# Optimization experiments

Measured on AMD Instinct MI355X. Metric: run time of the kernel, lower is better.

## Reference

```python
import jax, jax.numpy as jnp
import numpy as np

N = 100000
E = 1600000
IN_C, HID_C, OUT_C = 128, 128, 64


def setup_inputs() -> dict:
    key = jax.random.key(0)
    k_x, k_e, k_w1, k_w2 = jax.random.split(key, 4)
    x = jax.random.normal(k_x, (N, IN_C), dtype=jnp.float32)
    edge_index = jax.random.randint(k_e, (2, E), 0, N, dtype=jnp.int32)
    # nn.Linear default init: U(-1/sqrt(fan_in), 1/sqrt(fan_in)); bias init zeros per module
    lim1 = 1.0 / np.sqrt(IN_C)
    lim2 = 1.0 / np.sqrt(HID_C)
    W1 = jax.random.uniform(k_w1, (IN_C, HID_C), minval=-lim1, maxval=lim1, dtype=jnp.float32)
    b1 = jnp.zeros((HID_C,), dtype=jnp.float32)
    W2 = jax.random.uniform(k_w2, (HID_C, OUT_C), minval=-lim2, maxval=lim2, dtype=jnp.float32)
    b2 = jnp.zeros((OUT_C,), dtype=jnp.float32)
    return {"x": x, "edge_index": edge_index, "W1": W1, "b1": b1, "W2": W2, "b2": b2}


def _out_degree_gcn_conv(x, src, dst, W, b, n_nodes):
    # linear projection (no bias in lin)
    h = x @ W  # [N, out_c]
    # out-degree of each source node
    deg = jax.ops.segment_sum(jnp.ones((src.shape[0],), dtype=h.dtype), src, num_segments=n_nodes)
    deg_inv = 1.0 / jnp.maximum(deg, 1.0)  # clamp(min=1)
    h = h * deg_inv[:, None]
    # message: x_j = h[src]; aggregate: sum at dst
    out = jax.ops.segment_sum(h[src], dst, num_segments=n_nodes)  # [N, out_c]
    return out + b


def reference(x, edge_index, W1, b1, W2, b2):
    src, dst = edge_index[0], edge_index[1]
    n = x.shape[0]
    h = _out_degree_gcn_conv(x, src, dst, W1, b1, n)
    h = jax.nn.relu(h)
    # dropout p=0.0 -> identity
    out = _out_degree_gcn_conv(h, src, dst, W2, b2, n)
    return out
```

## Files before the change

### kernel.cpp

```cpp
#include <hip/hip_runtime.h>
#include <hip/hip_bf16.h>


typedef __attribute__((ext_vector_type(8))) short short8;
typedef __attribute__((ext_vector_type(4))) float floatx4;

__device__ inline unsigned short f2bf(float f) {
    union { float f; unsigned u; } v; v.f = f;
    unsigned r = v.u + 0x7FFF + ((v.u >> 16) & 1);
    return (unsigned short)(r >> 16);
}
__device__ inline float bf2f(unsigned b) {
    union { unsigned u; float f; } v; v.u = b << 16;
    return v.f;
}
__device__ inline float bf2f_hi(unsigned b) {
    union { unsigned u; float f; } v; v.u = b & 0xFFFF0000u;
    return v.f;
}

#define NBMAX 512
#define CAP   8192

__global__ __launch_bounds__(256) void convw_kernel(
    const float* __restrict__ W1, const float* __restrict__ W2,
    unsigned short* __restrict__ Wb1, unsigned short* __restrict__ Wb2,
    int* __restrict__ cnt)
{
    int i = blockIdx.x * 256 + threadIdx.x;
    if (i < NBMAX * 32) cnt[i] = 0;
    if (i < 128 * 128) {
        int k = i >> 7, n = i & 127;
        Wb1[n * 128 + k] = f2bf(W1[k * 128 + n]);
    }
    i -= 128 * 128;
    if (i >= 0 && i < 128 * 64) {
        int k = i >> 6, n = i & 63;
        Wb2[n * 128 + k] = f2bf(W2[k * 64 + n]);
    }
}

__global__ __launch_bounds__(256) void scatter2_kernel(
    const int* __restrict__ src, const int* __restrict__ dst, int E,
    int* __restrict__ cnt_d, int* __restrict__ cnt_s,
    unsigned* __restrict__ pairs, unsigned char* __restrict__ srcs_b, int NB)
{
    __shared__ int hd[NBMAX], bd[NBMAX], cd_[NBMAX];
    __shared__ int hs[NBMAX], bs[NBMAX], cs_[NBMAX];
    for (int i = threadIdx.x; i < NB; i += 256) { hd[i] = 0; cd_[i] = 0; hs[i] = 0; cs_[i] = 0; }
    __syncthreads();
    const int e0 = blockIdx.x * 8192;
    const int e1 = min(e0 + 8192, E);
    for (int i = e0 + threadIdx.x; i < e1; i += 256) {
        atomicAdd(&hd[dst[i] >> 8], 1);
        atomicAdd(&hs[src[i] >> 8], 1);
    }
    __syncthreads();
    for (int i = threadIdx.x; i < NB; i += 256) {
        if (hd[i]) bd[i] = atomicAdd(&cnt_d[i * 16], hd[i]);
        if (hs[i]) bs[i] = atomicAdd(&cnt_s[i * 16], hs[i]);
    }
    __syncthreads();
    for (int i = e0 + threadIdx.x; i < e1; i += 256) {
        int sv = src[i], dv = dst[i];
        int b = dv >> 8;
        int slot = atomicAdd(&cd_[b], 1);
        pairs[(size_t)b * CAP + bd[b] + slot] = ((unsigned)(dv & 255) << 24) | (unsigned)sv;
        int b2 = sv >> 8;
        int slot2 = atomicAdd(&cs_[b2], 1);
        srcs_b[(size_t)b2 * CAP + bs[b2] + slot2] = (unsigned char)(sv & 255);
    }
}

__global__ __launch_bounds__(256) void bucket_finalize_kernel(
    const unsigned* __restrict__ pairs, const unsigned char* __restrict__ srcs_b,
    const int* __restrict__ cnt_d, const int* __restrict__ cnt_s,
    int* __restrict__ sorted_src, int2* __restrict__ se,
    float* __restrict__ deg_inv, int N)
{
    const int b = blockIdx.x;
    const int node0 = b << 8;
    const int t = threadIdx.x;
    const size_t base = (size_t)b * CAP;
    __shared__ int hist[256];
    __shared__ int cur[256];
    __shared__ int pre[256];

    const int cd = cnt_d[b * 16];
    hist[t] = 0;
    __syncthreads();
    for (int i = t; i < cd; i += 256)
        atomicAdd(&hist[pairs[base + i] >> 24], 1);
    __syncthreads();
    int v = hist[t];
    int v4 = (v + 3) & ~3;
    pre[t] = v4;
    __syncthreads();
    for (int o = 1; o < 256; o <<= 1) {
        int add = (t >= o) ? pre[t - o] : 0;
        __syncthreads();
        pre[t] += add;
        __syncthreads();
    }
    int excl = pre[t] - v4;
    cur[t] = excl;
    if (node0 + t < N)
        se[node0 + t] = make_int2((int)base + excl, (int)base + excl + v);
    __syncthreads();
    for (int i = t; i < cd; i += 256) {
        unsigned p = pairs[base + i];
        int pos = atomicAdd(&cur[p >> 24], 1);
        sorted_src[base + pos] = (int)(p & 0xFFFFFFu);
    }

    __syncthreads();
    hist[t] = 0;
    __syncthreads();
    const int cs = cnt_s[b * 16];
    for (int i = t; i < cs; i += 256)
        atomicAdd(&hist[srcs_b[base + i]], 1);
    __syncthreads();
    if (node0 + t < N) {
        int d = hist[t];
        deg_inv[node0 + t] = 1.0f / (float)(d < 1 ? 1 : d);
    }
}

template <int NC, int AF>
__global__ __launch_bounds__(256) void gemm_mfma_kernel(
    const void* __restrict__ Ap, const unsigned short* __restrict__ Wb,
    const float* __restrict__ scale, unsigned short* __restrict__ Cb, int M)
{
    constexpr int NT = NC / 16;
    const int t = threadIdx.x;
    const int wm = t >> 6;
    const int lane = t & 63;
    const int lm = lane & 15;
    const int lk = (lane >> 4) * 8;

    const int r0 = blockIdx.x * 64 + wm * 16;
    int row = r0 + lm;
    if (row >= M) row = M - 1;

    floatx4 acc[NT];
#pragma unroll
    for (int j = 0; j < NT; ++j) acc[j] = (floatx4){0.f, 0.f, 0.f, 0.f};

#pragma unroll
    for (int kk = 0; kk < 4; ++kk) {
        const int kb = kk * 32 + lk;
        short8 af;
        if (AF) {
            const float* arow = (const float*)Ap + (size_t)row * 128 + kb;
            float4 a0 = *(const float4*)arow;
            float4 a1 = *(const float4*)(arow + 4);
            af[0] = (short)f2bf(a0.x); af[1] = (short)f2bf(a0.y);
            af[2] = (short)f2bf(a0.z); af[3] = (short)f2bf(a0.w);
            af[4] = (short)f2bf(a1.x); af[5] = (short)f2bf(a1.y);
            af[6] = (short)f2bf(a1.z); af[7] = (short)f2bf(a1.w);
        } else {
            af = *(const short8*)&((const unsigned short*)Ap)[(size_t)row * 128 + kb];
        }
#pragma unroll
        for (int j = 0; j < NT; ++j) {
            short8 bfr = *(const short8*)&Wb[(size_t)(j * 16 + lm) * 128 + kb];
            acc[j] = __builtin_amdgcn_mfma_f32_16x16x32_bf16(af, bfr, acc[j], 0, 0, 0);
        }
    }

    const int rbase = r0 + (lane >> 4) * 4;
#pragma unroll
    for (int reg = 0; reg < 4; ++reg) {
        int rg = rbase + reg;
        if (rg < M) {
            float di = AF ? scale[rg] : 1.0f;
#pragma unroll
            for (int j = 0; j < NT; ++j)
                Cb[(size_t)rg * NC + j * 16 + lm] = f2bf(AF ? acc[j][reg] * di : acc[j][reg]);
        }
    }
}

__global__ __launch_bounds__(256) void aggregate128_kernel(
    const int2* __restrict__ se, const int* __restrict__ sorted_src,
    const unsigned* __restrict__ val, const float* __restrict__ bias,
    const float* __restrict__ deg_inv, unsigned* __restrict__ outb, int N)
{
    int node = blockIdx.x * 8 + (threadIdx.x >> 5);
    if (node >= N) return;
    int l = threadIdx.x & 31;
    int2 r = se[node];
    int e = r.x;
    const int end = r.y;
    float a0 = 0.f, a1 = 0.f, a2 = 0.f, a3 = 0.f;
    if (e + 4 <= end) {
        int4 idx = *(const int4*)&sorted_src[e];
        for (; e + 8 <= end; e += 4) {
            int4 nidx = *(const int4*)&sorted_src[e + 4];
            uint2 v0 = *(const uint2*)&val[(size_t)idx.x * 64 + 2 * l];
            uint2 v1 = *(const uint2*)&val[(size_t)idx.y * 64 + 2 * l];
            uint2 v2 = *(const uint2*)&val[(size_t)idx.z * 64 + 2 * l];
            uint2 v3 = *(const uint2*)&val[(size_t)idx.w * 64 + 2 * l];
            a0 += (bf2f(v0.x & 0xFFFF) + bf2f(v1.x & 0xFFFF)) + (bf2f(v2.x & 0xFFFF) + bf2f(v3.x & 0xFFFF));
            a1 += (bf2f_hi(v0.x) + bf2f_hi(v1.x)) + (bf2f_hi(v2.x) + bf2f_hi(v3.x));
            a2 += (bf2f(v0.y & 0xFFFF) + bf2f(v1.y & 0xFFFF)) + (bf2f(v2.y & 0xFFFF) + bf2f(v3.y & 0xFFFF));
            a3 += (bf2f_hi(v0.y) + bf2f_hi(v1.y)) + (bf2f_hi(v2.y) + bf2f_hi(v3.y));
            idx = nidx;
        }
        uint2 v0 = *(const uint2*)&val[(size_t)idx.x * 64 + 2 * l];
        uint2 v1 = *(const uint2*)&val[(size_t)idx.y * 64 + 2 * l];
        uint2 v2 = *(const uint2*)&val[(size_t)idx.z * 64 + 2 * l];
        uint2 v3 = *(const uint2*)&val[(size_t)idx.w * 64 + 2 * l];
        a0 += (bf2f(v0.x & 0xFFFF) + bf2f(v1.x & 0xFFFF)) + (bf2f(v2.x & 0xFFFF) + bf2f(v3.x & 0xFFFF));
        a1 += (bf2f_hi(v0.x) + bf2f_hi(v1.x)) + (bf2f_hi(v2.x) + bf2f_hi(v3.x));
        a2 += (bf2f(v0.y & 0xFFFF) + bf2f(v1.y & 0xFFFF)) + (bf2f(v2.y & 0xFFFF) + bf2f(v3.y & 0xFFFF));
        a3 += (bf2f_hi(v0.y) + bf2f_hi(v1.y)) + (bf2f_hi(v2.y) + bf2f_hi(v3.y));
        e += 4;
    }
    for (; e < end; ++e) {
        uint2 v = *(const uint2*)&val[(size_t)sorted_src[e] * 64 + 2 * l];
        a0 += bf2f(v.x & 0xFFFF);
        a1 += bf2f_hi(v.x);
        a2 += bf2f(v.y & 0xFFFF);
        a3 += bf2f_hi(v.y);
    }
    float di = deg_inv[node];
    float4 bv = *(const float4*)&bias[4 * l];
    a0 = fmaxf(a0 + bv.x, 0.f) * di;
    a1 = fmaxf(a1 + bv.y, 0.f) * di;
    a2 = fmaxf(a2 + bv.z, 0.f) * di;
    a3 = fmaxf(a3 + bv.w, 0.f) * di;
    uint2 o;
    o.x = (unsigned)f2bf(a0) | ((unsigned)f2bf(a1) << 16);
    o.y = (unsigned)f2bf(a2) | ((unsigned)f2bf(a3) << 16);
    *(uint2*)&outb[(size_t)node * 64 + 2 * l] = o;
}

__global__ __launch_bounds__(256) void aggregate64_kernel(
    const int2* __restrict__ se, const int* __restrict__ sorted_src,
    const unsigned* __restrict__ val, const float* __restrict__ bias,
    float* __restrict__ out, int N)
{
    int node = blockIdx.x * 8 + (threadIdx.x >> 5);
    if (node >= N) return;
    int l = threadIdx.x & 31;
    int2 r = se[node];
    int e = r.x;
    const int end = r.y;
    float ax = 0.f, ay = 0.f;
    if (e + 4 <= end) {
        int4 idx = *(const int4*)&sorted_src[e];
        for (; e + 8 <= end; e += 4) {
            int4 nidx = *(const int4*)&sorted_src[e + 4];
            unsigned v0 = val[(size_t)idx.x * 32 + l];
            unsigned v1 = val[(size_t)idx.y * 32 + l];
            unsigned v2 = val[(size_t)idx.z * 32 + l];
            unsigned v3 = val[(size_t)idx.w * 32 + l];
            ax += (bf2f(v0 & 0xFFFF) + bf2f(v1 & 0xFFFF)) + (bf2f(v2 & 0xFFFF) + bf2f(v3 & 0xFFFF));
            ay += (bf2f_hi(v0) + bf2f_hi(v1)) + (bf2f_hi(v2) + bf2f_hi(v3));
            idx = nidx;
        }
        unsigned v0 = val[(size_t)idx.x * 32 + l];
        unsigned v1 = val[(size_t)idx.y * 32 + l];
        unsigned v2 = val[(size_t)idx.z * 32 + l];
        unsigned v3 = val[(size_t)idx.w * 32 + l];
        ax += (bf2f(v0 & 0xFFFF) + bf2f(v1 & 0xFFFF)) + (bf2f(v2 & 0xFFFF) + bf2f(v3 & 0xFFFF));
        ay += (bf2f_hi(v0) + bf2f_hi(v1)) + (bf2f_hi(v2) + bf2f_hi(v3));
        e += 4;
    }
    for (; e < end; ++e) {
        unsigned v = val[(size_t)sorted_src[e] * 32 + l];
        ax += bf2f(v & 0xFFFF);
        ay += bf2f_hi(v);
    }
    float2 o = make_float2(ax + bias[2 * l], ay + bias[2 * l + 1]);
    *(float2*)&out[(size_t)node * 64 + 2 * l] = o;
}

extern "C" void kernel_launch(void* const* d_in, const int* in_sizes, int n_in,
                              void* d_out, int out_size, void* d_ws, size_t ws_size,
                              hipStream_t stream) {
    const float* x  = (const float*)d_in[0];
    const int*   ei = (const int*)d_in[1];
    const float* W1 = (const float*)d_in[2];
    const float* b1 = (const float*)d_in[3];
    const float* W2 = (const float*)d_in[4];
    const float* b2 = (const float*)d_in[5];
    float* out = (float*)d_out;

    const int N = in_sizes[0] / 128;
    const int E = in_sizes[1] / 2;
    const int* src = ei;
    const int* dst = ei + E;
    const int NB = (N + 255) >> 8;

    char* ws = (char*)d_ws;
    size_t off = 0;
    auto alloc = [&](size_t bytes) {
        void* p = ws + off;
        off = (off + bytes + 255) & ~(size_t)255;
        return p;
    };
    float* deg_inv  = (float*)alloc((size_t)N * 4);
    int2*  se       = (int2*)alloc((size_t)N * 8);
    int*   cnt_d    = (int*)alloc((size_t)NBMAX * 16 * 4 * 2);
    int*   cnt_s    = cnt_d + (size_t)NBMAX * 16;
    unsigned short* Wb1 = (unsigned short*)alloc((size_t)128 * 128 * 2);
    unsigned short* Wb2 = (unsigned short*)alloc((size_t)64 * 128 * 2);
    unsigned*      pairs  = (unsigned*)alloc((size_t)NBMAX * CAP * 4);
    unsigned char* srcs_b = (unsigned char*)alloc((size_t)NBMAX * CAP);
    int*   sorted_src = (int*)alloc((size_t)NBMAX * CAP * 4);
    unsigned short* h    = (unsigned short*)alloc((size_t)N * 128 * 2);
    unsigned short* out1 = (unsigned short*)alloc((size_t)N * 128 * 2);
    unsigned short* g    = h;

    convw_kernel<<<96, 256, 0, stream>>>(W1, W2, Wb1, Wb2, cnt_d);
    scatter2_kernel<<<(E + 8191) / 8192, 256, 0, stream>>>(src, dst, E, cnt_d, cnt_s,
                                                           pairs, srcs_b, NB);
    bucket_finalize_kernel<<<NB, 256, 0, stream>>>(pairs, srcs_b, cnt_d, cnt_s,
                                                   sorted_src, se, deg_inv, N);

    const int gblocks = (N + 63) / 64;
    gemm_mfma_kernel<128, 1><<<gblocks, 256, 0, stream>>>(x, Wb1, deg_inv, h, N);
    aggregate128_kernel<<<(N + 7) / 8, 256, 0, stream>>>(se, sorted_src, (const unsigned*)h, b1,
                                                         deg_inv, (unsigned*)out1, N);
    gemm_mfma_kernel<64, 0><<<gblocks, 256, 0, stream>>>(out1, Wb2, nullptr, g, N);
    aggregate64_kernel<<<(N + 7) / 8, 256, 0, stream>>>(se, sorted_src, (const unsigned*)g, b2, out, N);
}
```

Before: 309.4 us.

## Pad per-node edge lists to multiples of four with a zero sentinel row

The bucket finalize kernel now fills the padding slots of each node's edge segment (already rounded to multiples of 4) with index N. The GEMM kernels write a zero row at index N of their output, so padded gathers add zero. The aggregation loops then drop the scalar tail loop and process 8 edges per iteration with all loads issued together, which raises memory-level parallelism. The layer-2 GEMM output moves into the reused pairs buffer so it does not overwrite h, and the extra sentinel gathers add some wasted loads.

```diff
diff --git a/kernel.cpp b/kernel.cpp
--- a/kernel.cpp
+++ b/kernel.cpp
@@ -104,8 +104,10 @@
     }
     int excl = pre[t] - v4;
     cur[t] = excl;
-    if (node0 + t < N)
+    if (node0 + t < N) {
         se[node0 + t] = make_int2((int)base + excl, (int)base + excl + v);
+        for (int i = v; i < v4; ++i) sorted_src[base + excl + i] = N;
+    }
     __syncthreads();
     for (int i = t; i < cd; i += 256) {
         unsigned p = pairs[base + i];
@@ -133,6 +135,8 @@
 {
     constexpr int NT = NC / 16;
     const int t = threadIdx.x;
+    if (blockIdx.x == 0 && t < NC / 2)
+        ((unsigned*)Cb)[(size_t)M * (NC / 2) + t] = 0;
     const int wm = t >> 6;
     const int lane = t & 63;
     const int lm = lane & 15;
@@ -181,6 +185,27 @@
     }
 }
 
+#define LD128(vv, ii) uint2 vv = *(const uint2*)&val[(size_t)(ii) * 64 + 2 * l]
+#define ACC8_128(I0, I1) do { \
+    LD128(v0, I0.x); LD128(v1, I0.y); LD128(v2, I0.z); LD128(v3, I0.w); \
+    LD128(v4, I1.x); LD128(v5, I1.y); LD128(v6, I1.z); LD128(v7, I1.w); \
+    a0 += ((bf2f(v0.x & 0xFFFF) + bf2f(v1.x & 0xFFFF)) + (bf2f(v2.x & 0xFFFF) + bf2f(v3.x & 0xFFFF))) \
+        + ((bf2f(v4.x & 0xFFFF) + bf2f(v5.x & 0xFFFF)) + (bf2f(v6.x & 0xFFFF) + bf2f(v7.x & 0xFFFF))); \
+    a1 += ((bf2f_hi(v0.x) + bf2f_hi(v1.x)) + (bf2f_hi(v2.x) + bf2f_hi(v3.x))) \
+        + ((bf2f_hi(v4.x) + bf2f_hi(v5.x)) + (bf2f_hi(v6.x) + bf2f_hi(v7.x))); \
+    a2 += ((bf2f(v0.y & 0xFFFF) + bf2f(v1.y & 0xFFFF)) + (bf2f(v2.y & 0xFFFF) + bf2f(v3.y & 0xFFFF))) \
+        + ((bf2f(v4.y & 0xFFFF) + bf2f(v5.y & 0xFFFF)) + (bf2f(v6.y & 0xFFFF) + bf2f(v7.y & 0xFFFF))); \
+    a3 += ((bf2f_hi(v0.y) + bf2f_hi(v1.y)) + (bf2f_hi(v2.y) + bf2f_hi(v3.y))) \
+        + ((bf2f_hi(v4.y) + bf2f_hi(v5.y)) + (bf2f_hi(v6.y) + bf2f_hi(v7.y))); \
+} while (0)
+#define ACC4_128(I0) do { \
+    LD128(v0, I0.x); LD128(v1, I0.y); LD128(v2, I0.z); LD128(v3, I0.w); \
+    a0 += (bf2f(v0.x & 0xFFFF) + bf2f(v1.x & 0xFFFF)) + (bf2f(v2.x & 0xFFFF) + bf2f(v3.x & 0xFFFF)); \
+    a1 += (bf2f_hi(v0.x) + bf2f_hi(v1.x)) + (bf2f_hi(v2.x) + bf2f_hi(v3.x)); \
+    a2 += (bf2f(v0.y & 0xFFFF) + bf2f(v1.y & 0xFFFF)) + (bf2f(v2.y & 0xFFFF) + bf2f(v3.y & 0xFFFF)); \
+    a3 += (bf2f_hi(v0.y) + bf2f_hi(v1.y)) + (bf2f_hi(v2.y) + bf2f_hi(v3.y)); \
+} while (0)
+
 __global__ __launch_bounds__(256) void aggregate128_kernel(
     const int2* __restrict__ se, const int* __restrict__ sorted_src,
     const unsigned* __restrict__ val, const float* __restrict__ bias,
@@ -191,39 +216,26 @@
     int l = threadIdx.x & 31;
     int2 r = se[node];
     int e = r.x;
-    const int end = r.y;
+    const int end4 = r.x + ((r.y - r.x + 3) & ~3);
     float a0 = 0.f, a1 = 0.f, a2 = 0.f, a3 = 0.f;
-    if (e + 4 <= end) {
-        int4 idx = *(const int4*)&sorted_src[e];
-        for (; e + 8 <= end; e += 4) {
-            int4 nidx = *(const int4*)&sorted_src[e + 4];
-            uint2 v0 = *(const uint2*)&val[(size_t)idx.x * 64 + 2 * l];
-            uint2 v1 = *(const uint2*)&val[(size_t)idx.y * 64 + 2 * l];
-            uint2 v2 = *(const uint2*)&val[(size_t)idx.z * 64 + 2 * l];
-            uint2 v3 = *(const uint2*)&val[(size_t)idx.w * 64 + 2 * l];
-            a0 += (bf2f(v0.x & 0xFFFF) + bf2f(v1.x & 0xFFFF)) + (bf2f(v2.x & 0xFFFF) + bf2f(v3.x & 0xFFFF));
-            a1 += (bf2f_hi(v0.x) + bf2f_hi(v1.x)) + (bf2f_hi(v2.x) + bf2f_hi(v3.x));
-            a2 += (bf2f(v0.y & 0xFFFF) + bf2f(v1.y & 0xFFFF)) + (bf2f(v2.y & 0xFFFF) + bf2f(v3.y & 0xFFFF));
-            a3 += (bf2f_hi(v0.y) + bf2f_hi(v1.y)) + (bf2f_hi(v2.y) + bf2f_hi(v3.y));
-            idx = nidx;
-        }
-        uint2 v0 = *(const uint2*)&val[(size_t)idx.x * 64 + 2 * l];
-        uint2 v1 = *(const uint2*)&val[(size_t)idx.y * 64 + 2 * l];
-        uint2 v2 = *(const uint2*)&val[(size_t)idx.z * 64 + 2 * l];
-        uint2 v3 = *(const uint2*)&val[(size_t)idx.w * 64 + 2 * l];
-        a0 += (bf2f(v0.x & 0xFFFF) + bf2f(v1.x & 0xFFFF)) + (bf2f(v2.x & 0xFFFF) + bf2f(v3.x & 0xFFFF));
-        a1 += (bf2f_hi(v0.x) + bf2f_hi(v1.x)) + (bf2f_hi(v2.x) + bf2f_hi(v3.x));
-        a2 += (bf2f(v0.y & 0xFFFF) + bf2f(v1.y & 0xFFFF)) + (bf2f(v2.y & 0xFFFF) + bf2f(v3.y & 0xFFFF));
-        a3 += (bf2f_hi(v0.y) + bf2f_hi(v1.y)) + (bf2f_hi(v2.y) + bf2f_hi(v3.y));
-        e += 4;
-    }
-    for (; e < end; ++e) {
-        uint2 v = *(const uint2*)&val[(size_t)sorted_src[e] * 64 + 2 * l];
-        a0 += bf2f(v.x & 0xFFFF);
-        a1 += bf2f_hi(v.x);
-        a2 += bf2f(v.y & 0xFFFF);
-        a3 += bf2f_hi(v.y);
-    }
+
+    if (e + 8 <= end4) {
+        int4 i0 = *(const int4*)&sorted_src[e];
+        int4 i1 = *(const int4*)&sorted_src[e + 4];
+        for (; e + 16 <= end4; e += 8) {
+            int4 n0 = *(const int4*)&sorted_src[e + 8];
+            int4 n1 = *(const int4*)&sorted_src[e + 12];
+            ACC8_128(i0, i1);
+            i0 = n0; i1 = n1;
+        }
+        ACC8_128(i0, i1);
+        e += 8;
+    }
+    if (e < end4) {
+        int4 i0 = *(const int4*)&sorted_src[e];
+        ACC4_128(i0);
+    }
+
     float di = deg_inv[node];
     float4 bv = *(const float4*)&bias[4 * l];
     a0 = fmaxf(a0 + bv.x, 0.f) * di;
@@ -236,6 +248,21 @@
     *(uint2*)&outb[(size_t)node * 64 + 2 * l] = o;
 }
 
+#define LD64(vv, ii) unsigned vv = val[(size_t)(ii) * 32 + l]
+#define ACC8_64(I0, I1) do { \
+    LD64(v0, I0.x); LD64(v1, I0.y); LD64(v2, I0.z); LD64(v3, I0.w); \
+    LD64(v4, I1.x); LD64(v5, I1.y); LD64(v6, I1.z); LD64(v7, I1.w); \
+    ax += ((bf2f(v0 & 0xFFFF) + bf2f(v1 & 0xFFFF)) + (bf2f(v2 & 0xFFFF) + bf2f(v3 & 0xFFFF))) \
+        + ((bf2f(v4 & 0xFFFF) + bf2f(v5 & 0xFFFF)) + (bf2f(v6 & 0xFFFF) + bf2f(v7 & 0xFFFF))); \
+    ay += ((bf2f_hi(v0) + bf2f_hi(v1)) + (bf2f_hi(v2) + bf2f_hi(v3))) \
+        + ((bf2f_hi(v4) + bf2f_hi(v5)) + (bf2f_hi(v6) + bf2f_hi(v7))); \
+} while (0)
+#define ACC4_64(I0) do { \
+    LD64(v0, I0.x); LD64(v1, I0.y); LD64(v2, I0.z); LD64(v3, I0.w); \
+    ax += (bf2f(v0 & 0xFFFF) + bf2f(v1 & 0xFFFF)) + (bf2f(v2 & 0xFFFF) + bf2f(v3 & 0xFFFF)); \
+    ay += (bf2f_hi(v0) + bf2f_hi(v1)) + (bf2f_hi(v2) + bf2f_hi(v3)); \
+} while (0)
+
 __global__ __launch_bounds__(256) void aggregate64_kernel(
     const int2* __restrict__ se, const int* __restrict__ sorted_src,
     const unsigned* __restrict__ val, const float* __restrict__ bias,
@@ -246,33 +273,26 @@
     int l = threadIdx.x & 31;
     int2 r = se[node];
     int e = r.x;
-    const int end = r.y;
+    const int end4 = r.x + ((r.y - r.x + 3) & ~3);
     float ax = 0.f, ay = 0.f;
-    if (e + 4 <= end) {
-        int4 idx = *(const int4*)&sorted_src[e];
-        for (; e + 8 <= end; e += 4) {
-            int4 nidx = *(const int4*)&sorted_src[e + 4];
-            unsigned v0 = val[(size_t)idx.x * 32 + l];
-            unsigned v1 = val[(size_t)idx.y * 32 + l];
-            unsigned v2 = val[(size_t)idx.z * 32 + l];
-            unsigned v3 = val[(size_t)idx.w * 32 + l];
-            ax += (bf2f(v0 & 0xFFFF) + bf2f(v1 & 0xFFFF)) + (bf2f(v2 & 0xFFFF) + bf2f(v3 & 0xFFFF));
-            ay += (bf2f_hi(v0) + bf2f_hi(v1)) + (bf2f_hi(v2) + bf2f_hi(v3));
-            idx = nidx;
-        }
-        unsigned v0 = val[(size_t)idx.x * 32 + l];
-        unsigned v1 = val[(size_t)idx.y * 32 + l];
-        unsigned v2 = val[(size_t)idx.z * 32 + l];
-        unsigned v3 = val[(size_t)idx.w * 32 + l];
-        ax += (bf2f(v0 & 0xFFFF) + bf2f(v1 & 0xFFFF)) + (bf2f(v2 & 0xFFFF) + bf2f(v3 & 0xFFFF));
-        ay += (bf2f_hi(v0) + bf2f_hi(v1)) + (bf2f_hi(v2) + bf2f_hi(v3));
-        e += 4;
-    }
-    for (; e < end; ++e) {
-        unsigned v = val[(size_t)sorted_src[e] * 32 + l];
-        ax += bf2f(v & 0xFFFF);
-        ay += bf2f_hi(v);
-    }
+
+    if (e + 8 <= end4) {
+        int4 i0 = *(const int4*)&sorted_src[e];
+        int4 i1 = *(const int4*)&sorted_src[e + 4];
+        for (; e + 16 <= end4; e += 8) {
+            int4 n0 = *(const int4*)&sorted_src[e + 8];
+            int4 n1 = *(const int4*)&sorted_src[e + 12];
+            ACC8_64(i0, i1);
+            i0 = n0; i1 = n1;
+        }
+        ACC8_64(i0, i1);
+        e += 8;
+    }
+    if (e < end4) {
+        int4 i0 = *(const int4*)&sorted_src[e];
+        ACC4_64(i0);
+    }
+
     float2 o = make_float2(ax + bias[2 * l], ay + bias[2 * l + 1]);
     *(float2*)&out[(size_t)node * 64 + 2 * l] = o;
 }
@@ -310,9 +330,11 @@
     unsigned*      pairs  = (unsigned*)alloc((size_t)NBMAX * CAP * 4);
     unsigned char* srcs_b = (unsigned char*)alloc((size_t)NBMAX * CAP);
     int*   sorted_src = (int*)alloc((size_t)NBMAX * CAP * 4);
-    unsigned short* h    = (unsigned short*)alloc((size_t)N * 128 * 2);
+    unsigned short* h    = (unsigned short*)alloc((size_t)(N + 1) * 128 * 2);
     unsigned short* out1 = (unsigned short*)alloc((size_t)N * 128 * 2);
-    unsigned short* g    = h;
+    unsigned short* g = ((size_t)(N + 1) * 128 <= (size_t)NBMAX * CAP * 4)
+                            ? (unsigned short*)pairs
+                            : (unsigned short*)alloc((size_t)(N + 1) * 64 * 2);
 
     convw_kernel<<<96, 256, 0, stream>>>(W1, W2, Wb1, Wb2, cnt_d);
     scatter2_kernel<<<(E + 8191) / 8192, 256, 0, stream>>>(src, dst, E, cnt_d, cnt_s,
```

New measurement: 302.4 us. -2.3%, faster.
